# Optimization experiments

Hardware: AMD Instinct MI355X
Metric: run time of the kernel (lower is better)

The kernel has to match this reference:

```python
import jax, jax.numpy as jnp
import numpy as np

CLASS_DIM = 4   # hardcoded in DsFunction1
PROTO_DIM = 20  # hardcoded in DsFunction1


def setup_inputs() -> dict:
    key = jax.random.key(0)
    k1, k2, k3 = jax.random.split(key, 3)
    B, C, H, Wd, D = 2, 16, 64, 64, 64
    inp = jax.random.normal(k1, (B, C, H, Wd, D), dtype=jnp.float32)
    W = jax.random.normal(k2, (PROTO_DIM, C), dtype=jnp.float32)
    BETA = jax.random.normal(k3, (PROTO_DIM, CLASS_DIM), dtype=jnp.float32) * 0.5
    alpha = jnp.zeros((PROTO_DIM, 1), dtype=jnp.float32)           # init 0 per reset_parameters
    gamma = jnp.full((PROTO_DIM, 1), 0.1, dtype=jnp.float32)       # init 0.1 per reset_parameters
    return {"input": inp, "W": W, "BETA": BETA, "alpha": alpha, "gamma": gamma}


def _ds_forward(x, W, BETA, alpha, gamma):
    # x: [B,C,H,Wd,D]; W: [K,C]; BETA: [K,M]; alpha, gamma: [K,1]
    B, C, H, Wd, D = x.shape
    BETA2 = BETA * BETA
    U = BETA2 / jnp.sum(BETA2, axis=1, keepdims=True)              # [K,M] membership weights
    alphap = 0.99 / (1.0 + jnp.exp(-alpha[:, 0]))                  # [K]

    # squared distances to prototypes: d[k] = 0.5 * ||x - W_k||^2 over channel dim
    x2 = jnp.sum(x * x, axis=1)                                    # [B,H,Wd,D]
    xw = jnp.einsum('bchwd,kc->kbhwd', x, W)                       # [K,B,H,Wd,D]
    w2 = jnp.sum(W * W, axis=1)                                    # [K]
    d = 0.5 * (x2[None] - 2.0 * xw + w2[:, None, None, None, None])  # [K,B,H,Wd,D]

    g2 = (gamma[:, 0] ** 2)[:, None, None, None, None]
    s = alphap[:, None, None, None, None] * jnp.exp(-g2 * d)       # [K,B,H,Wd,D]

    mfoc = U[:, :, None, None, None, None] * s[:, None]            # [K,M,B,H,Wd,D] focal masses
    momega = 1.0 - s                                               # [K,B,H,Wd,D] mass on Omega

    # sequential Dempster (unnormalized conjunctive) combination over prototypes
    def step(carry, km):
        mk_f, mk_o = carry                                         # [M,B,H,Wd,D], [B,H,Wd,D]
        m_f, m_o = km
        new_f = mk_f * (m_f + m_o[None]) + m_f * mk_o[None]
        new_o = mk_o * m_o
        return (new_f, new_o), None

    init = (jnp.zeros((CLASS_DIM, B, H, Wd, D), x.dtype),
            jnp.ones((B, H, Wd, D), x.dtype))
    (mk_f, mk_o), _ = jax.lax.scan(step, init, (mfoc, momega))

    mk = jnp.concatenate([mk_f, mk_o[None]], axis=0)               # [M+1,B,H,Wd,D]
    mk_n = mk / jnp.sum(mk, axis=0, keepdims=True)                 # normalize masses
    return jnp.transpose(mk_n, (1, 0, 2, 3, 4))                    # [B,M+1,H,Wd,D]


def reference(input, W, BETA, alpha, gamma):
    return _ds_forward(input, W, BETA, alpha, gamma)
```

## Files before the change

### kernel.cpp

```cpp
#include <hip/hip_runtime.h>
#include <hip/hip_bf16.h>
#include <math.h>

#define NK 20
#define NC 16
#define NM 4
#define TSTEP 4

typedef __attribute__((ext_vector_type(8)))  short  short8;
typedef __attribute__((ext_vector_type(16))) float  floatx16;

static __device__ __forceinline__ short bf16b(float f) {
    __hip_bfloat16 h = __float2bfloat16(f);
    return *reinterpret_cast<short*>(&h);
}

__global__ void ds_prep(const float* __restrict__ Wg,
                        const float* __restrict__ BETAg,
                        const float* __restrict__ alphag,
                        const float* __restrict__ gammag,
                        float* __restrict__ ws)
{
    const int p = threadIdx.x;
    if (p >= 32) return;
    float* cst = ws;
    short* Wpb = (short*)(ws + 256);
    short* A2b = (short*)(ws + 512);
    if (p < NK) {
        const float L   = 1.4426950408889634f;
        const float g   = gammag[p];
        const float g2L = g * g * L;
        float w2 = 0.f;
        #pragma unroll
        for (int c = 0; c < NC; ++c) {
            const float w = Wg[p*NC + c];
            Wpb[p*NC + c] = bf16b(g2L * w);
            w2 = fmaf(w, w, w2);
        }
        const float a = 0.99f / (1.0f + __expf(-alphag[p]));
        float b0 = BETAg[p*NM+0], b1 = BETAg[p*NM+1], b2 = BETAg[p*NM+2], b3 = BETAg[p*NM+3];
        b0 *= b0; b1 *= b1; b2 *= b2; b3 *= b3;
        const float uinv = 1.0f / (b0 + b1 + b2 + b3);
        cst[p*8+0] = (1.0f - b0*uinv) * a;
        cst[p*8+1] = (1.0f - b1*uinv) * a;
        cst[p*8+2] = (1.0f - b2*uinv) * a;
        cst[p*8+3] = (1.0f - b3*uinv) * a;
        cst[p*8+4] = a;
        cst[p*8+5] = 0.f; cst[p*8+6] = 0.f; cst[p*8+7] = 0.f;
        A2b[p*2+0] = bf16b(-0.5f * g2L);
        A2b[p*2+1] = bf16b(-0.5f * g2L * w2);
    } else {
        #pragma unroll
        for (int i = 0; i < 8; ++i) cst[p*8+i] = 0.f;
        #pragma unroll
        for (int c = 0; c < NC; ++c) Wpb[p*NC + c] = 0;
        A2b[p*2+0] = 0; A2b[p*2+1] = 0;
    }
}

__global__ __launch_bounds__(256, 4) void ds_main(
    const float* __restrict__ inp,
    const float* __restrict__ ws,
    float* __restrict__ out,
    int S,
    int BS)
{
    const int lane = threadIdx.x & 63;
    const int half = lane >> 5;
    const int col  = lane & 31;
    const int gw   = blockIdx.x * 4 + (threadIdx.x >> 6);

    const float* cst = ws;
    const short* Wpb = (const short*)(ws + 256);
    const short* A2b = (const short*)(ws + 512);

    const short8 afrag = *(const short8*)(Wpb + col*NC + half*8);
    short8 a2frag;
    #pragma unroll
    for (int j = 0; j < 8; ++j) a2frag[j] = 0;
    if (half == 0) { a2frag[0] = A2b[col*2+0]; a2frag[1] = A2b[col*2+1]; }

    float cm0[12], cm1[12], cm2[12], cm3[12], cO[12];
    #pragma unroll
    for (int r = 0; r < 12; ++r) {
        const int p = (r & 3) + 8*(r >> 2) + 4*half;
        const float4 cv = *(const float4*)(cst + p*8);
        cm0[r] = cv.x; cm1[r] = cv.y; cm2[r] = cv.z; cm3[r] = cv.w;
        cO[r]  = cst[p*8 + 4];
    }

    #pragma unroll
    for (int t = 0; t < TSTEP; ++t) {
        const int base = (gw * TSTEP + t) * 32;
        if (base >= BS) break;
        const int e  = base + col;
        const int b  = (e >= S) ? 1 : 0;
        const int sp = e - b * S;
        const float* xb = inp + (size_t)b * NC * S + sp;

        short8 bfrag;
        float x2p = 0.f;
        #pragma unroll
        for (int j = 0; j < 8; ++j) {
            const float v = xb[(size_t)(8*half + j) * S];
            x2p = fmaf(v, v, x2p);
            bfrag[j] = bf16b(v);
        }
        const float x2 = x2p + __shfl_xor(x2p, 32, 64);

        short8 b2frag;
        #pragma unroll
        for (int j = 0; j < 8; ++j) b2frag[j] = 0;
        if (half == 0) { b2frag[0] = bf16b(x2); b2frag[1] = (short)0x3F80; }

        floatx16 acc;
        #pragma unroll
        for (int i = 0; i < 16; ++i) acc[i] = 0.f;
        acc = __builtin_amdgcn_mfma_f32_32x32x16_bf16(afrag,  bfrag,  acc, 0, 0, 0);
        acc = __builtin_amdgcn_mfma_f32_32x32x16_bf16(a2frag, b2frag, acc, 0, 0, 0);

        float P0 = 1.f, P1 = 1.f, P2 = 1.f, P3 = 1.f, PO = 1.f;
        #pragma unroll
        for (int r = 0; r < 12; ++r) {
            const float ek = __builtin_amdgcn_exp2f(acc[r]);
            P0 *= fmaf(-cm0[r], ek, 1.0f);
            P1 *= fmaf(-cm1[r], ek, 1.0f);
            P2 *= fmaf(-cm2[r], ek, 1.0f);
            P3 *= fmaf(-cm3[r], ek, 1.0f);
            PO *= fmaf(-cO[r],  ek, 1.0f);
        }
        P0 *= __shfl_xor(P0, 32, 64);
        P1 *= __shfl_xor(P1, 32, 64);
        P2 *= __shfl_xor(P2, 32, 64);
        P3 *= __shfl_xor(P3, 32, 64);
        PO *= __shfl_xor(PO, 32, 64);

        const float O  = PO;
        const float f0 = P0 - O, f1 = P1 - O, f2 = P2 - O, f3 = P3 - O;
        const float inv = 1.0f / (f0 + f1 + f2 + f3 + O);
        if (half == 0) {
            float* op = out + (size_t)b * (NM+1) * S + sp;
            op[0]            = f0 * inv;
            op[(size_t)S]    = f1 * inv;
            op[(size_t)2*S]  = f2 * inv;
            op[(size_t)3*S]  = f3 * inv;
            op[(size_t)4*S]  = O  * inv;
        }
    }
}

extern "C" void kernel_launch(void* const* d_in, const int* in_sizes, int n_in,
                              void* d_out, int out_size, void* d_ws, size_t ws_size,
                              hipStream_t stream) {
    const float* inp   = (const float*)d_in[0];
    const float* Wg    = (const float*)d_in[1];
    const float* BETAg = (const float*)d_in[2];
    const float* alphag= (const float*)d_in[3];
    const float* gammag= (const float*)d_in[4];
    float* out = (float*)d_out;
    float* ws  = (float*)d_ws;

    const int BS = in_sizes[0] / NC;
    const int S  = BS / 2;

    ds_prep<<<1, 64, 0, stream>>>(Wg, BETAg, alphag, gammag, ws);

    const int elems_per_block = 4 * TSTEP * 32;
    const int grid = (BS + elems_per_block - 1) / elems_per_block;
    ds_main<<<grid, 256, 0, stream>>>(inp, ws, out, S, BS);
}
```

Baseline: 86.47 us.

## Fuse prep into main kernel and prefetch input before MFMA loop

Drops the separate single-block prep launch; each block now recomputes the prototype constants into shared memory and synchronises once. All input loads for the warp are issued up front, before the constant setup and MFMA loop, to hide memory latency. TSTEP drops to 2, which doubles the grid, and the output stores are split across both half-waves. The cost is redundant per-block constant computation and a __syncthreads, and the bounds check on the tail is removed.

```diff
diff --git a/kernel.cpp b/kernel.cpp
--- a/kernel.cpp
+++ b/kernel.cpp
@@ -5,7 +5,7 @@
 #define NK 20
 #define NC 16
 #define NM 4
-#define TSTEP 4
+#define TSTEP 2
 
 typedef __attribute__((ext_vector_type(8)))  short  short8;
 typedef __attribute__((ext_vector_type(16))) float  floatx16;
@@ -15,94 +15,95 @@
     return *reinterpret_cast<short*>(&h);
 }
 
-__global__ void ds_prep(const float* __restrict__ Wg,
-                        const float* __restrict__ BETAg,
-                        const float* __restrict__ alphag,
-                        const float* __restrict__ gammag,
-                        float* __restrict__ ws)
-{
-    const int p = threadIdx.x;
-    if (p >= 32) return;
-    float* cst = ws;
-    short* Wpb = (short*)(ws + 256);
-    short* A2b = (short*)(ws + 512);
-    if (p < NK) {
-        const float L   = 1.4426950408889634f;
-        const float g   = gammag[p];
-        const float g2L = g * g * L;
-        float w2 = 0.f;
-        #pragma unroll
-        for (int c = 0; c < NC; ++c) {
-            const float w = Wg[p*NC + c];
-            Wpb[p*NC + c] = bf16b(g2L * w);
-            w2 = fmaf(w, w, w2);
-        }
-        const float a = 0.99f / (1.0f + __expf(-alphag[p]));
-        float b0 = BETAg[p*NM+0], b1 = BETAg[p*NM+1], b2 = BETAg[p*NM+2], b3 = BETAg[p*NM+3];
-        b0 *= b0; b1 *= b1; b2 *= b2; b3 *= b3;
-        const float uinv = 1.0f / (b0 + b1 + b2 + b3);
-        cst[p*8+0] = (1.0f - b0*uinv) * a;
-        cst[p*8+1] = (1.0f - b1*uinv) * a;
-        cst[p*8+2] = (1.0f - b2*uinv) * a;
-        cst[p*8+3] = (1.0f - b3*uinv) * a;
-        cst[p*8+4] = a;
-        cst[p*8+5] = 0.f; cst[p*8+6] = 0.f; cst[p*8+7] = 0.f;
-        A2b[p*2+0] = bf16b(-0.5f * g2L);
-        A2b[p*2+1] = bf16b(-0.5f * g2L * w2);
-    } else {
-        #pragma unroll
-        for (int i = 0; i < 8; ++i) cst[p*8+i] = 0.f;
-        #pragma unroll
-        for (int c = 0; c < NC; ++c) Wpb[p*NC + c] = 0;
-        A2b[p*2+0] = 0; A2b[p*2+1] = 0;
-    }
-}
-
-__global__ __launch_bounds__(256, 4) void ds_main(
+__global__ __launch_bounds__(256, 4) void ds_fused(
     const float* __restrict__ inp,
-    const float* __restrict__ ws,
+    const float* __restrict__ Wg,
+    const float* __restrict__ BETAg,
+    const float* __restrict__ alphag,
+    const float* __restrict__ gammag,
     float* __restrict__ out,
     int S,
     int BS)
 {
-    const int lane = threadIdx.x & 63;
+    __shared__ __align__(16) float sCst[32][8];
+    __shared__ __align__(16) short sWpb[32][16];
+    __shared__ short sA2[32][2];
+
+    const int t = threadIdx.x;
+    if (t < 32) {
+        if (t < NK) {
+            const float L   = 1.4426950408889634f;
+            const float g   = gammag[t];
+            const float g2L = g * g * L;
+            float w2 = 0.f;
+            #pragma unroll
+            for (int c = 0; c < NC; ++c) {
+                const float w = Wg[t*NC + c];
+                sWpb[t][c] = bf16b(g2L * w);
+                w2 = fmaf(w, w, w2);
+            }
+            const float a = 0.99f / (1.0f + __expf(-alphag[t]));
+            float b0 = BETAg[t*NM+0], b1 = BETAg[t*NM+1], b2 = BETAg[t*NM+2], b3 = BETAg[t*NM+3];
+            b0 *= b0; b1 *= b1; b2 *= b2; b3 *= b3;
+            const float uinv = 1.0f / (b0 + b1 + b2 + b3);
+            sCst[t][0] = (1.0f - b0*uinv) * a;
+            sCst[t][1] = (1.0f - b1*uinv) * a;
+            sCst[t][2] = (1.0f - b2*uinv) * a;
+            sCst[t][3] = (1.0f - b3*uinv) * a;
+            sCst[t][4] = a;
+            sCst[t][5] = 0.f; sCst[t][6] = 0.f; sCst[t][7] = 0.f;
+            sA2[t][0] = bf16b(-0.5f * g2L);
+            sA2[t][1] = bf16b(-0.5f * g2L * w2);
+        } else {
+            #pragma unroll
+            for (int i = 0; i < 8; ++i) sCst[t][i] = 0.f;
+            #pragma unroll
+            for (int c = 0; c < NC; ++c) sWpb[t][c] = 0;
+            sA2[t][0] = 0; sA2[t][1] = 0;
+        }
+    }
+    __syncthreads();
+
+    const int lane = t & 63;
     const int half = lane >> 5;
     const int col  = lane & 31;
-    const int gw   = blockIdx.x * 4 + (threadIdx.x >> 6);
+    const int gw   = blockIdx.x * 4 + (t >> 6);
+    const int ebase = gw * (TSTEP * 32);
 
-    const float* cst = ws;
-    const short* Wpb = (const short*)(ws + 256);
-    const short* A2b = (const short*)(ws + 512);
+    const int b  = (ebase >= S) ? 1 : 0;
+    const int spw = ebase - b * S;
+    const float* xb0 = inp + (size_t)b * NC * S + spw + col;
+    float xv[TSTEP][8];
+    #pragma unroll
+    for (int tt = 0; tt < TSTEP; ++tt)
+        #pragma unroll
+        for (int j = 0; j < 8; ++j)
+            xv[tt][j] = xb0[(size_t)(8*half + j) * S + tt*32];
 
-    const short8 afrag = *(const short8*)(Wpb + col*NC + half*8);
+    const short8 afrag = *(const short8*)&sWpb[col][half*8];
     short8 a2frag;
     #pragma unroll
     for (int j = 0; j < 8; ++j) a2frag[j] = 0;
-    if (half == 0) { a2frag[0] = A2b[col*2+0]; a2frag[1] = A2b[col*2+1]; }
+    if (half == 0) { a2frag[0] = sA2[col][0]; a2frag[1] = sA2[col][1]; }
 
     float cm0[12], cm1[12], cm2[12], cm3[12], cO[12];
     #pragma unroll
     for (int r = 0; r < 12; ++r) {
         const int p = (r & 3) + 8*(r >> 2) + 4*half;
-        const float4 cv = *(const float4*)(cst + p*8);
+        const float4 cv = *(const float4*)&sCst[p][0];
         cm0[r] = cv.x; cm1[r] = cv.y; cm2[r] = cv.z; cm3[r] = cv.w;
-        cO[r]  = cst[p*8 + 4];
+        cO[r]  = sCst[p][4];
     }
 
     #pragma unroll
-    for (int t = 0; t < TSTEP; ++t) {
-        const int base = (gw * TSTEP + t) * 32;
-        if (base >= BS) break;
-        const int e  = base + col;
-        const int b  = (e >= S) ? 1 : 0;
-        const int sp = e - b * S;
-        const float* xb = inp + (size_t)b * NC * S + sp;
+    for (int tt = 0; tt < TSTEP; ++tt) {
+        const int sp = spw + tt*32 + col;
 
         short8 bfrag;
         float x2p = 0.f;
         #pragma unroll
         for (int j = 0; j < 8; ++j) {
-            const float v = xb[(size_t)(8*half + j) * S];
+            const float v = xv[tt][j];
             x2p = fmaf(v, v, x2p);
             bfrag[j] = bf16b(v);
         }
@@ -138,13 +139,15 @@
         const float O  = PO;
         const float f0 = P0 - O, f1 = P1 - O, f2 = P2 - O, f3 = P3 - O;
         const float inv = 1.0f / (f0 + f1 + f2 + f3 + O);
+
+        float* op = out + (size_t)b * (NM+1) * S + sp;
         if (half == 0) {
-            float* op = out + (size_t)b * (NM+1) * S + sp;
-            op[0]            = f0 * inv;
-            op[(size_t)S]    = f1 * inv;
-            op[(size_t)2*S]  = f2 * inv;
-            op[(size_t)3*S]  = f3 * inv;
-            op[(size_t)4*S]  = O  * inv;
+            op[0]           = f0 * inv;
+            op[(size_t)S]   = f1 * inv;
+            op[(size_t)2*S] = f2 * inv;
+        } else {
+            op[(size_t)3*S] = f3 * inv;
+            op[(size_t)4*S] = O  * inv;
         }
     }
 }
@@ -158,14 +161,11 @@
     const float* alphag= (const float*)d_in[3];
     const float* gammag= (const float*)d_in[4];
     float* out = (float*)d_out;
-    float* ws  = (float*)d_ws;
 
     const int BS = in_sizes[0] / NC;
     const int S  = BS / 2;
 
-    ds_prep<<<1, 64, 0, stream>>>(Wg, BETAg, alphag, gammag, ws);
-
     const int elems_per_block = 4 * TSTEP * 32;
     const int grid = (BS + elems_per_block - 1) / elems_per_block;
-    ds_main<<<grid, 256, 0, stream>>>(inp, ws, out, S, BS);
+    ds_fused<<<grid, 256, 0, stream>>>(inp, Wg, BETAg, alphag, gammag, out, S, BS);
 }
```

Result: no change. 85.61 us (-1.0%).
